# Kernel optimization log

Hardware: AMD Instinct MI355X
Metric: run time of the kernel (lower is better)

## Reference

```python
import jax, jax.numpy as jnp
import numpy as np
from jax import lax

B, T, C_IN, H, K = 8, 4096, 256, 256, 3


def _conv1d_same(x_nct, w_oik, b_o):
    # x: [B, C, T], w: [H, C, K], b: [H] -> [B, H, T], 'same' padding
    y = lax.conv_general_dilated(x_nct, w_oik, window_strides=(1,),
                                 padding='SAME',
                                 dimension_numbers=('NCH', 'OIH', 'NCH'))
    return y + b_o[None, :, None]


def setup_inputs() -> dict:
    key = jax.random.key(0)
    ks = jax.random.split(key, 7)
    std = 1.0 / np.sqrt(H)
    u = lambda k, shape: jax.random.uniform(k, shape, jnp.float32, -std, std)
    return {
        'inputs': jax.random.normal(ks[0], (B, T, C_IN), jnp.float32),
        'init_f': jax.random.normal(ks[1], (B, H), jnp.float32),
        'init_z': jax.random.normal(ks[2], (B, H), jnp.float32),
        'f_w': u(ks[3], (H, C_IN, K)),
        'f_b': u(ks[4], (H,)),
        'z_w': u(ks[5], (H, C_IN, K)),
        'z_b': u(ks[6], (H,)),
    }


def reference(inputs, init_f, init_z, f_w, f_b, z_w, z_b):
    x = jnp.transpose(inputs, (0, 2, 1))                    # [B, C, T]
    raw_f = jnp.transpose(_conv1d_same(x, f_w, f_b), (0, 2, 1))  # [B, T, H]
    raw_z = jnp.transpose(_conv1d_same(x, z_w, z_b), (0, 2, 1))
    # prepend init state along time: init_state[0] -> f, init_state[1] -> z
    raw_f = jnp.concatenate([init_f[:, None, :], raw_f], axis=1)  # [B, T+1, H]
    raw_z = jnp.concatenate([init_z[:, None, :], raw_z], axis=1)
    log_one_minus_f = jax.nn.log_sigmoid(-raw_f)
    log_z = jax.nn.log_sigmoid(raw_z)
    log_f = jax.nn.log_sigmoid(raw_f)
    cs = jnp.cumsum(log_f, axis=1)
    recurrent_gates = log_f - cs + cs[:, -1:, :]
    log_hidden = lax.cumlogsumexp(log_z + log_one_minus_f + recurrent_gates, axis=1)
    return jnp.exp(log_hidden - recurrent_gates)            # [B, T+1, H]
```

## Files before the change

kernel.cpp:

```cpp
#include <hip/hip_runtime.h>
#include <hip/hip_bf16.h>

#define B_ 8
#define T_ 4096
#define C_ 256
#define H_ 256
#define K_ 3
#define NC 128
#define TC 32
#define WFRAG_ELEMS (24 * 32 * 64 * 8)

typedef __attribute__((ext_vector_type(8))) __bf16 bf16x8;
typedef __attribute__((ext_vector_type(4))) float f32x4;

__device__ __forceinline__ float sigm(float x) { return 1.0f / (1.0f + __expf(-x)); }

__device__ __forceinline__ ushort f2bf(float f) {
    union { float f; unsigned u; } v; v.f = f;
    return (ushort)((v.u + 0x7FFFu + ((v.u >> 16) & 1u)) >> 16);
}
__device__ __forceinline__ float bf2f(ushort u) {
    union { unsigned u; float f; } v; v.u = ((unsigned)u) << 16; return v.f;
}
__device__ __forceinline__ unsigned cvt_pk_bf16(float lo, float hi) {
    unsigned r;
    asm("v_cvt_pk_bf16_f32 %0, %1, %2" : "=v"(r) : "v"(lo), "v"(hi));
    return r;
}

__global__ __launch_bounds__(256) void wfrag_kernel(const float* __restrict__ fw,
                                                    const float* __restrict__ zw,
                                                    ushort* __restrict__ wfrag) {
    int idx = blockIdx.x * 256 + threadIdx.x;
    if (idx >= WFRAG_ELEMS) return;
    int j   = idx & 7;
    int l   = (idx >> 3) & 63;
    int ntg = (idx >> 9) & 31;
    int ks  = idx >> 14;
    int n = ntg * 16 + (l & 15);
    int kappa = ks * 32 + (l >> 4) * 8 + j;
    int k = kappa >> 8, c = kappa & 255;
    const float* w = (n < 256) ? fw : zw;
    int h = n & 255;
    wfrag[idx] = f2bf(w[(h * C_ + c) * K_ + k]);
}

__device__ __forceinline__ void bload(const ushort* wb, int ks, const int (&ntg)[4],
                                      bf16x8 (&dst)[4]) {
#pragma unroll
    for (int ni = 0; ni < 4; ++ni)
        dst[ni] = *(const bf16x8*)(wb + (size_t)ks * 16384 + (size_t)ntg[ni] * 512);
}

__device__ __forceinline__ void conv_step(const char* smem, int ks, int lr, int lg,
                                          const bf16x8 (&bfr)[4], f32x4 (&acc)[4][4]) {
    const int k = ks >> 3;
    const int cb = ((ks & 7) * 32 + lg * 8) * 2;
    bf16x8 afr[4];
#pragma unroll
    for (int mi = 0; mi < 4; ++mi) {
        int row = mi * 16 + lr + k;
        afr[mi] = *(const bf16x8*)(smem + row * 512 + (cb ^ ((row & 7) << 4)));
    }
    __builtin_amdgcn_s_setprio(1);
#pragma unroll
    for (int ni = 0; ni < 4; ++ni)
#pragma unroll
        for (int mi = 0; mi < 4; ++mi)
            acc[mi][ni] = __builtin_amdgcn_mfma_f32_16x16x32_bf16(afr[mi], bfr[ni], acc[mi][ni], 0, 0, 0);
    __builtin_amdgcn_s_setprio(0);
}

__global__ __launch_bounds__(512, 4) void conv_scan_kernel(const float* __restrict__ x,
                                                           const ushort* __restrict__ wfrag,
                                                           const float* __restrict__ fb,
                                                           const float* __restrict__ zb,
                                                           unsigned* __restrict__ AP,
                                                           float2* __restrict__ ab) {
    __shared__ __align__(16) char smem[65536];
    unsigned* buf = (unsigned*)smem;

    const int b = blockIdx.y;
    const int t0 = blockIdx.x * 64;
    const int tid = threadIdx.x;

    if (blockIdx.x == 0 || blockIdx.x == gridDim.x - 1) {
        for (int idx = tid; idx < 66 * 64; idx += 512) {
            int row = idx >> 6;
            int c4 = (idx & 63) * 4;
            int t = t0 - 1 + row;
            float4 v = make_float4(0.f, 0.f, 0.f, 0.f);
            if (t >= 0 && t < T_) v = *(const float4*)(x + ((size_t)(b * T_ + t)) * C_ + c4);
            uint2 w2 = make_uint2(cvt_pk_bf16(v.x, v.y), cvt_pk_bf16(v.z, v.w));
            *(uint2*)(smem + row * 512 + ((c4 * 2) ^ ((row & 7) << 4))) = w2;
        }
    } else {
        for (int idx = tid; idx < 66 * 64; idx += 512) {
            int row = idx >> 6;
            int c4 = (idx & 63) * 4;
            int t = t0 - 1 + row;
            float4 v = *(const float4*)(x + ((size_t)(b * T_ + t)) * C_ + c4);
            uint2 w2 = make_uint2(cvt_pk_bf16(v.x, v.y), cvt_pk_bf16(v.z, v.w));
            *(uint2*)(smem + row * 512 + ((c4 * 2) ^ ((row & 7) << 4))) = w2;
        }
    }
    __syncthreads();

    const int wv = tid >> 6;
    const int l  = tid & 63;
    const int lr = l & 15;
    const int lg = l >> 4;
    const int h0 = wv * 32;

    f32x4 acc[4][4];
#pragma unroll
    for (int ni = 0; ni < 4; ++ni) {
        float bv = (ni < 2 ? fb : zb)[h0 + (ni & 1) * 16 + lr];
        f32x4 bvv = {bv, bv, bv, bv};
#pragma unroll
        for (int mi = 0; mi < 4; ++mi) acc[mi][ni] = bvv;
    }

    const ushort* wb = wfrag + (size_t)l * 8;
    int ntg_[4];
#pragma unroll
    for (int ni = 0; ni < 4; ++ni)
        ntg_[ni] = (ni < 2) ? (wv * 2 + ni) : (16 + wv * 2 + ni - 2);

    bf16x8 ba[4], bb[4];
    bload(wb, 0, ntg_, ba);
#pragma unroll 1
    for (int ks = 0; ks < 24; ks += 2) {
        bload(wb, ks + 1, ntg_, bb);
        conv_step(smem, ks, lr, lg, ba, acc);
        if (ks + 2 < 24) bload(wb, ks + 2, ntg_, ba);
        conv_step(smem, ks + 1, lr, lg, bb, acc);
    }

    __syncthreads();
#pragma unroll
    for (int mi = 0; mi < 4; ++mi) {
#pragma unroll
        for (int ni = 0; ni < 2; ++ni) {
            const int h = h0 + ni * 16 + lr;
#pragma unroll
            for (int r = 0; r < 4; ++r) {
                float fv = sigm(acc[mi][ni][r]);
                float av = sigm(acc[mi][ni + 2][r]) * (1.0f - fv);
                int tl = (mi & 1) * 16 + lg * 4 + r;
                int trow = (mi >> 1) * 32 + tl;
                buf[trow * 256 + (h ^ ((tl << 2) & 31))] = cvt_pk_bf16(av, fv);
            }
        }
    }
    __syncthreads();

    {
        const int ch = tid >> 8;
        const int h = tid & 255;
        const int chunk = blockIdx.x * 2 + ch;
        const int r0 = chunk * TC;
        const unsigned* bp = buf + ch * 32 * 256;
        unsigned* app = AP + ((size_t)b * T_ + r0) * H_ + h;
        unsigned u = bp[h];
        float A = bf2f((ushort)(u & 0xffff));
        float Pp = 1.0f;
        float f_prev = bf2f((ushort)(u >> 16));
        app[0] = cvt_pk_bf16(A, Pp);
#pragma unroll 8
        for (int j = 1; j < TC; ++j) {
            u = bp[j * 256 + (h ^ ((j << 2) & 31))];
            float a = bf2f((ushort)(u & 0xffff));
            float f = bf2f((ushort)(u >> 16));
            A = fmaf(f_prev, A, a);
            Pp *= f_prev;
            f_prev = f;
            app[(size_t)j * H_] = cvt_pk_bf16(A, Pp);
        }
        ab[((size_t)b * NC + chunk) * H_ + h] = make_float2(f_prev * A, f_prev * Pp);
    }
}

__global__ __launch_bounds__(256) void chainapply_kernel(const unsigned* __restrict__ AP,
                                                         const float2* __restrict__ ab,
                                                         const float* __restrict__ init_f,
                                                         const float* __restrict__ init_z,
                                                         float* __restrict__ out) {
    const int p = blockIdx.x;
    const int tq = p >> 3;
    const int c = 16 * (tq >> 1) + 2 * (p & 7) + (tq & 1);
    const int b = blockIdx.y;
    const int h = threadIdx.x;

    float f0 = sigm(init_f[b * H_ + h]);
    float z0 = sigm(init_z[b * H_ + h]);
    float s0 = z0 * (1.0f - f0);
    if (c == 0) out[(size_t)b * (T_ + 1) * H_ + h] = s0;

    float uv = f0 * s0;
    const float2* abp = ab + (size_t)b * NC * H_ + h;
#pragma unroll 8
    for (int cc = 0; cc < c; ++cc) {
        float2 q = abp[(size_t)cc * H_];
        uv = fmaf(q.y, uv, q.x);
    }

    const unsigned* app = AP + ((size_t)b * T_ + c * TC) * H_ + h;
    float* op = out + ((size_t)b * (T_ + 1) + c * TC + 1) * H_ + h;
#pragma unroll 8
    for (int j = 0; j < TC; ++j) {
        unsigned w = app[(size_t)j * H_];
        op[(size_t)j * H_] = fmaf(bf2f((ushort)(w >> 16)), uv, bf2f((ushort)(w & 0xffff)));
    }
}

extern "C" void kernel_launch(void* const* d_in, const int* in_sizes, int n_in,
                              void* d_out, int out_size, void* d_ws, size_t ws_size,
                              hipStream_t stream) {
    const float* inputs = (const float*)d_in[0];
    const float* init_f = (const float*)d_in[1];
    const float* init_z = (const float*)d_in[2];
    const float* f_w    = (const float*)d_in[3];
    const float* f_b    = (const float*)d_in[4];
    const float* z_w    = (const float*)d_in[5];
    const float* z_b    = (const float*)d_in[6];
    float* out = (float*)d_out;

    ushort* wfrag = (ushort*)d_ws;
    unsigned* AP  = (unsigned*)(wfrag + WFRAG_ELEMS);
    float2* ab    = (float2*)(AP + (size_t)B_ * T_ * H_);

    wfrag_kernel<<<(WFRAG_ELEMS + 255) / 256, 256, 0, stream>>>(f_w, z_w, wfrag);

    dim3 cgrid(T_ / 64, B_, 1);
    conv_scan_kernel<<<cgrid, 512, 0, stream>>>(inputs, wfrag, f_b, z_b, AP, ab);

    dim3 agrid(NC, B_, 1);
    chainapply_kernel<<<agrid, 256, 0, stream>>>(AP, ab, init_f, init_z, out);
}
```

Baseline: 64.79 us.

## Double conv tile to 128 timesteps per block to reuse weight fragments

Each conv block now processes 128 timesteps with two accumulator sets, so every weight fragment loaded from global feeds twice as many MFMAs. The epilogue scans the result in two passes through shared memory, and chainapply's chunk ordering is remapped to match. Dynamic shared memory grows to hold the larger input halo. The cost is more accumulator registers and lower occupancy (launch bound 2), plus a grid of only 256 blocks, which may underfill the GPU.

```diff
diff --git a/kernel.cpp b/kernel.cpp
--- a/kernel.cpp
+++ b/kernel.cpp
@@ -8,7 +8,9 @@
 #define K_ 3
 #define NC 128
 #define TC 32
+#define BM 128
 #define WFRAG_ELEMS (24 * 32 * 64 * 8)
+#define SMEM_BYTES 66560
 
 typedef __attribute__((ext_vector_type(8))) __bf16 bf16x8;
 typedef __attribute__((ext_vector_type(4))) float f32x4;
@@ -52,40 +54,46 @@
         dst[ni] = *(const bf16x8*)(wb + (size_t)ks * 16384 + (size_t)ntg[ni] * 512);
 }
 
-__device__ __forceinline__ void conv_step(const char* smem, int ks, int lr, int lg,
-                                          const bf16x8 (&bfr)[4], f32x4 (&acc)[4][4]) {
+__device__ __forceinline__ void conv_step2(const char* smem, int ks, int lr, int lg,
+                                           const bf16x8 (&bfr)[4], f32x4 (&acc)[2][4][4]) {
     const int k = ks >> 3;
     const int cb = ((ks & 7) * 32 + lg * 8) * 2;
-    bf16x8 afr[4];
-#pragma unroll
-    for (int mi = 0; mi < 4; ++mi) {
-        int row = mi * 16 + lr + k;
-        afr[mi] = *(const bf16x8*)(smem + row * 512 + (cb ^ ((row & 7) << 4)));
-    }
+    bf16x8 afr[2][4];
+#pragma unroll
+    for (int tt = 0; tt < 2; ++tt)
+#pragma unroll
+        for (int mi = 0; mi < 4; ++mi) {
+            int row = tt * 64 + mi * 16 + lr + k;
+            afr[tt][mi] = *(const bf16x8*)(smem + row * 512 + (cb ^ ((row & 7) << 4)));
+        }
     __builtin_amdgcn_s_setprio(1);
 #pragma unroll
     for (int ni = 0; ni < 4; ++ni)
 #pragma unroll
-        for (int mi = 0; mi < 4; ++mi)
-            acc[mi][ni] = __builtin_amdgcn_mfma_f32_16x16x32_bf16(afr[mi], bfr[ni], acc[mi][ni], 0, 0, 0);
+        for (int tt = 0; tt < 2; ++tt)
+#pragma unroll
+            for (int mi = 0; mi < 4; ++mi)
+                acc[tt][mi][ni] = __builtin_amdgcn_mfma_f32_16x16x32_bf16(afr[tt][mi], bfr[ni],
+                                                                          acc[tt][mi][ni], 0, 0, 0);
     __builtin_amdgcn_s_setprio(0);
 }
 
-__global__ __launch_bounds__(512, 4) void conv_scan_kernel(const float* __restrict__ x,
+__global__ __launch_bounds__(512, 2) void conv_scan_kernel(const float* __restrict__ x,
                                                            const ushort* __restrict__ wfrag,
                                                            const float* __restrict__ fb,
                                                            const float* __restrict__ zb,
                                                            unsigned* __restrict__ AP,
                                                            float2* __restrict__ ab) {
-    __shared__ __align__(16) char smem[65536];
+    extern __shared__ __align__(16) char smem[];
     unsigned* buf = (unsigned*)smem;
 
     const int b = blockIdx.y;
-    const int t0 = blockIdx.x * 64;
+    const int bx = blockIdx.x;
+    const int t0 = bx * BM;
     const int tid = threadIdx.x;
 
-    if (blockIdx.x == 0 || blockIdx.x == gridDim.x - 1) {
-        for (int idx = tid; idx < 66 * 64; idx += 512) {
+    if (bx == 0 || bx == gridDim.x - 1) {
+        for (int idx = tid; idx < 130 * 64; idx += 512) {
             int row = idx >> 6;
             int c4 = (idx & 63) * 4;
             int t = t0 - 1 + row;
@@ -95,7 +103,7 @@
             *(uint2*)(smem + row * 512 + ((c4 * 2) ^ ((row & 7) << 4))) = w2;
         }
     } else {
-        for (int idx = tid; idx < 66 * 64; idx += 512) {
+        for (int idx = tid; idx < 130 * 64; idx += 512) {
             int row = idx >> 6;
             int c4 = (idx & 63) * 4;
             int t = t0 - 1 + row;
@@ -112,13 +120,15 @@
     const int lg = l >> 4;
     const int h0 = wv * 32;
 
-    f32x4 acc[4][4];
+    f32x4 acc[2][4][4];
 #pragma unroll
     for (int ni = 0; ni < 4; ++ni) {
         float bv = (ni < 2 ? fb : zb)[h0 + (ni & 1) * 16 + lr];
         f32x4 bvv = {bv, bv, bv, bv};
 #pragma unroll
-        for (int mi = 0; mi < 4; ++mi) acc[mi][ni] = bvv;
+        for (int tt = 0; tt < 2; ++tt)
+#pragma unroll
+            for (int mi = 0; mi < 4; ++mi) acc[tt][mi][ni] = bvv;
     }
 
     const ushort* wb = wfrag + (size_t)l * 8;
@@ -132,33 +142,34 @@
 #pragma unroll 1
     for (int ks = 0; ks < 24; ks += 2) {
         bload(wb, ks + 1, ntg_, bb);
-        conv_step(smem, ks, lr, lg, ba, acc);
+        conv_step2(smem, ks, lr, lg, ba, acc);
         if (ks + 2 < 24) bload(wb, ks + 2, ntg_, ba);
-        conv_step(smem, ks + 1, lr, lg, bb, acc);
-    }
-
-    __syncthreads();
-#pragma unroll
-    for (int mi = 0; mi < 4; ++mi) {
-#pragma unroll
-        for (int ni = 0; ni < 2; ++ni) {
-            const int h = h0 + ni * 16 + lr;
-#pragma unroll
-            for (int r = 0; r < 4; ++r) {
-                float fv = sigm(acc[mi][ni][r]);
-                float av = sigm(acc[mi][ni + 2][r]) * (1.0f - fv);
-                int tl = (mi & 1) * 16 + lg * 4 + r;
-                int trow = (mi >> 1) * 32 + tl;
-                buf[trow * 256 + (h ^ ((tl << 2) & 31))] = cvt_pk_bf16(av, fv);
+        conv_step2(smem, ks + 1, lr, lg, bb, acc);
+    }
+
+#pragma unroll 1
+    for (int p = 0; p < 2; ++p) {
+        __syncthreads();
+#pragma unroll
+        for (int mi = 0; mi < 4; ++mi) {
+#pragma unroll
+            for (int ni = 0; ni < 2; ++ni) {
+                const int h = h0 + ni * 16 + lr;
+#pragma unroll
+                for (int r = 0; r < 4; ++r) {
+                    float fv = sigm(acc[p][mi][ni][r]);
+                    float av = sigm(acc[p][mi][ni + 2][r]) * (1.0f - fv);
+                    int tl = (mi & 1) * 16 + lg * 4 + r;
+                    int trow = (mi >> 1) * 32 + tl;
+                    buf[trow * 256 + (h ^ ((tl << 2) & 31))] = cvt_pk_bf16(av, fv);
+                }
             }
         }
-    }
-    __syncthreads();
-
-    {
+        __syncthreads();
+
         const int ch = tid >> 8;
         const int h = tid & 255;
-        const int chunk = blockIdx.x * 2 + ch;
+        const int chunk = bx * 4 + 2 * p + ch;
         const int r0 = chunk * TC;
         const unsigned* bp = buf + ch * 32 * 256;
         unsigned* app = AP + ((size_t)b * T_ + r0) * H_ + h;
@@ -187,8 +198,8 @@
                                                          const float* __restrict__ init_z,
                                                          float* __restrict__ out) {
     const int p = blockIdx.x;
-    const int tq = p >> 3;
-    const int c = 16 * (tq >> 1) + 2 * (p & 7) + (tq & 1);
+    const int q = p >> 3;
+    const int c = 4 * ((p & 7) + 8 * (q >> 2)) + (q & 3);
     const int b = blockIdx.y;
     const int h = threadIdx.x;
 
@@ -201,8 +212,8 @@
     const float2* abp = ab + (size_t)b * NC * H_ + h;
 #pragma unroll 8
     for (int cc = 0; cc < c; ++cc) {
-        float2 q = abp[(size_t)cc * H_];
-        uv = fmaf(q.y, uv, q.x);
+        float2 qv = abp[(size_t)cc * H_];
+        uv = fmaf(qv.y, uv, qv.x);
     }
 
     const unsigned* app = AP + ((size_t)b * T_ + c * TC) * H_ + h;
@@ -232,8 +243,10 @@
 
     wfrag_kernel<<<(WFRAG_ELEMS + 255) / 256, 256, 0, stream>>>(f_w, z_w, wfrag);
 
-    dim3 cgrid(T_ / 64, B_, 1);
-    conv_scan_kernel<<<cgrid, 512, 0, stream>>>(inputs, wfrag, f_b, z_b, AP, ab);
+    hipFuncSetAttribute((const void*)conv_scan_kernel,
+                        hipFuncAttributeMaxDynamicSharedMemorySize, SMEM_BYTES);
+    dim3 cgrid(T_ / BM, B_, 1);
+    conv_scan_kernel<<<cgrid, 512, SMEM_BYTES, stream>>>(inputs, wfrag, f_b, z_b, AP, ab);
 
     dim3 agrid(NC, B_, 1);
     chainapply_kernel<<<agrid, 256, 0, stream>>>(AP, ab, init_f, init_z, out);
```

New measurement: 85.02 us. 1.31x slower.

## Split conv-scan blocks across hidden halves and software-pipeline LDS A loads

Applied to the files above, without the earlier changes.

The conv+scan kernel now runs with 256 threads per block and a third grid dimension that splits the hidden units into two halves. This doubles the block count and shrinks shared memory to the 66-row input tile, allowing more resident blocks. The A-fragment LDS loads are double-buffered alongside the B loads so they overlap the MFMAs. The epilogue and per-chunk scan run in two phases that reuse the smaller buffer. Each time tile of input is now loaded and converted twice (once per half), and only 128 of 256 threads take part in the scan.

```diff
diff --git a/kernel.cpp b/kernel.cpp
--- a/kernel.cpp
+++ b/kernel.cpp
@@ -52,16 +52,19 @@
         dst[ni] = *(const bf16x8*)(wb + (size_t)ks * 16384 + (size_t)ntg[ni] * 512);
 }
 
-__device__ __forceinline__ void conv_step(const char* smem, int ks, int lr, int lg,
-                                          const bf16x8 (&bfr)[4], f32x4 (&acc)[4][4]) {
+__device__ __forceinline__ void aload(const char* smem, int ks, int lr, int lg,
+                                      bf16x8 (&afr)[4]) {
     const int k = ks >> 3;
     const int cb = ((ks & 7) * 32 + lg * 8) * 2;
-    bf16x8 afr[4];
 #pragma unroll
     for (int mi = 0; mi < 4; ++mi) {
         int row = mi * 16 + lr + k;
         afr[mi] = *(const bf16x8*)(smem + row * 512 + (cb ^ ((row & 7) << 4)));
     }
+}
+
+__device__ __forceinline__ void mfma_step(const bf16x8 (&afr)[4], const bf16x8 (&bfr)[4],
+                                          f32x4 (&acc)[4][4]) {
     __builtin_amdgcn_s_setprio(1);
 #pragma unroll
     for (int ni = 0; ni < 4; ++ni)
@@ -71,21 +74,70 @@
     __builtin_amdgcn_s_setprio(0);
 }
 
-__global__ __launch_bounds__(512, 4) void conv_scan_kernel(const float* __restrict__ x,
+template <int P>
+__device__ __forceinline__ void epi_write(f32x4 (&acc)[4][4], unsigned* buf,
+                                          int lr, int lg, int h0l) {
+#pragma unroll
+    for (int m2 = 0; m2 < 2; ++m2) {
+        const int mi = 2 * P + m2;
+#pragma unroll
+        for (int ni = 0; ni < 2; ++ni) {
+            const int hl = h0l + ni * 16 + lr;
+#pragma unroll
+            for (int r = 0; r < 4; ++r) {
+                float fv = sigm(acc[mi][ni][r]);
+                float av = sigm(acc[mi][ni + 2][r]) * (1.0f - fv);
+                int tl = m2 * 16 + lg * 4 + r;
+                buf[tl * 128 + (hl ^ ((tl << 2) & 31))] = cvt_pk_bf16(av, fv);
+            }
+        }
+    }
+}
+
+template <int P>
+__device__ __forceinline__ void chunk_scan(const unsigned* buf, int b, int bx, int hh,
+                                           int tid, unsigned* AP, float2* ab) {
+    if (tid < 128) {
+        const int hl = tid;
+        const int hg = hh * 128 + hl;
+        const int chunk = bx * 2 + P;
+        unsigned* app = AP + ((size_t)b * T_ + chunk * TC) * H_ + hg;
+        unsigned u = buf[hl];
+        float A = bf2f((ushort)(u & 0xffff));
+        float Pp = 1.0f;
+        float f_prev = bf2f((ushort)(u >> 16));
+        app[0] = cvt_pk_bf16(A, Pp);
+#pragma unroll 8
+        for (int j = 1; j < TC; ++j) {
+            u = buf[j * 128 + (hl ^ ((j << 2) & 31))];
+            float a = bf2f((ushort)(u & 0xffff));
+            float f = bf2f((ushort)(u >> 16));
+            A = fmaf(f_prev, A, a);
+            Pp *= f_prev;
+            f_prev = f;
+            app[(size_t)j * H_] = cvt_pk_bf16(A, Pp);
+        }
+        ab[((size_t)b * NC + chunk) * H_ + hg] = make_float2(f_prev * A, f_prev * Pp);
+    }
+}
+
+__global__ __launch_bounds__(256, 3) void conv_scan_kernel(const float* __restrict__ x,
                                                            const ushort* __restrict__ wfrag,
                                                            const float* __restrict__ fb,
                                                            const float* __restrict__ zb,
                                                            unsigned* __restrict__ AP,
                                                            float2* __restrict__ ab) {
-    __shared__ __align__(16) char smem[65536];
+    __shared__ __align__(16) char smem[66 * 512];
     unsigned* buf = (unsigned*)smem;
 
     const int b = blockIdx.y;
-    const int t0 = blockIdx.x * 64;
+    const int bx = blockIdx.x;
+    const int hh = blockIdx.z;
+    const int t0 = bx * 64;
     const int tid = threadIdx.x;
 
-    if (blockIdx.x == 0 || blockIdx.x == gridDim.x - 1) {
-        for (int idx = tid; idx < 66 * 64; idx += 512) {
+    if (bx == 0 || bx == gridDim.x - 1) {
+        for (int idx = tid; idx < 66 * 64; idx += 256) {
             int row = idx >> 6;
             int c4 = (idx & 63) * 4;
             int t = t0 - 1 + row;
@@ -95,7 +147,7 @@
             *(uint2*)(smem + row * 512 + ((c4 * 2) ^ ((row & 7) << 4))) = w2;
         }
     } else {
-        for (int idx = tid; idx < 66 * 64; idx += 512) {
+        for (int idx = tid; idx < 66 * 64; idx += 256) {
             int row = idx >> 6;
             int c4 = (idx & 63) * 4;
             int t = t0 - 1 + row;
@@ -110,12 +162,13 @@
     const int l  = tid & 63;
     const int lr = l & 15;
     const int lg = l >> 4;
-    const int h0 = wv * 32;
+    const int h0l = wv * 32;
+    const int h0g = hh * 128 + h0l;
 
     f32x4 acc[4][4];
 #pragma unroll
     for (int ni = 0; ni < 4; ++ni) {
-        float bv = (ni < 2 ? fb : zb)[h0 + (ni & 1) * 16 + lr];
+        float bv = (ni < 2 ? fb : zb)[h0g + (ni & 1) * 16 + lr];
         f32x4 bvv = {bv, bv, bv, bv};
 #pragma unroll
         for (int mi = 0; mi < 4; ++mi) acc[mi][ni] = bvv;
@@ -125,60 +178,32 @@
     int ntg_[4];
 #pragma unroll
     for (int ni = 0; ni < 4; ++ni)
-        ntg_[ni] = (ni < 2) ? (wv * 2 + ni) : (16 + wv * 2 + ni - 2);
-
-    bf16x8 ba[4], bb[4];
+        ntg_[ni] = (ni < 2) ? (hh * 8 + wv * 2 + ni) : (16 + hh * 8 + wv * 2 + ni - 2);
+
+    bf16x8 aA[4], aB[4], ba[4], bb[4];
     bload(wb, 0, ntg_, ba);
+    aload(smem, 0, lr, lg, aA);
 #pragma unroll 1
     for (int ks = 0; ks < 24; ks += 2) {
         bload(wb, ks + 1, ntg_, bb);
-        conv_step(smem, ks, lr, lg, ba, acc);
-        if (ks + 2 < 24) bload(wb, ks + 2, ntg_, ba);
-        conv_step(smem, ks + 1, lr, lg, bb, acc);
-    }
-
-    __syncthreads();
-#pragma unroll
-    for (int mi = 0; mi < 4; ++mi) {
-#pragma unroll
-        for (int ni = 0; ni < 2; ++ni) {
-            const int h = h0 + ni * 16 + lr;
-#pragma unroll
-            for (int r = 0; r < 4; ++r) {
-                float fv = sigm(acc[mi][ni][r]);
-                float av = sigm(acc[mi][ni + 2][r]) * (1.0f - fv);
-                int tl = (mi & 1) * 16 + lg * 4 + r;
-                int trow = (mi >> 1) * 32 + tl;
-                buf[trow * 256 + (h ^ ((tl << 2) & 31))] = cvt_pk_bf16(av, fv);
-            }
-        }
-    }
-    __syncthreads();
-
-    {
-        const int ch = tid >> 8;
-        const int h = tid & 255;
-        const int chunk = blockIdx.x * 2 + ch;
-        const int r0 = chunk * TC;
-        const unsigned* bp = buf + ch * 32 * 256;
-        unsigned* app = AP + ((size_t)b * T_ + r0) * H_ + h;
-        unsigned u = bp[h];
-        float A = bf2f((ushort)(u & 0xffff));
-        float Pp = 1.0f;
-        float f_prev = bf2f((ushort)(u >> 16));
-        app[0] = cvt_pk_bf16(A, Pp);
-#pragma unroll 8
-        for (int j = 1; j < TC; ++j) {
-            u = bp[j * 256 + (h ^ ((j << 2) & 31))];
-            float a = bf2f((ushort)(u & 0xffff));
-            float f = bf2f((ushort)(u >> 16));
-            A = fmaf(f_prev, A, a);
-            Pp *= f_prev;
-            f_prev = f;
-            app[(size_t)j * H_] = cvt_pk_bf16(A, Pp);
-        }
-        ab[((size_t)b * NC + chunk) * H_ + h] = make_float2(f_prev * A, f_prev * Pp);
-    }
+        aload(smem, ks + 1, lr, lg, aB);
+        mfma_step(aA, ba, acc);
+        if (ks + 2 < 24) {
+            bload(wb, ks + 2, ntg_, ba);
+            aload(smem, ks + 2, lr, lg, aA);
+        }
+        mfma_step(aB, bb, acc);
+    }
+
+    __syncthreads();
+    epi_write<0>(acc, buf, lr, lg, h0l);
+    __syncthreads();
+    chunk_scan<0>(buf, b, bx, hh, tid, AP, ab);
+
+    __syncthreads();
+    epi_write<1>(acc, buf, lr, lg, h0l);
+    __syncthreads();
+    chunk_scan<1>(buf, b, bx, hh, tid, AP, ab);
 }
 
 __global__ __launch_bounds__(256) void chainapply_kernel(const unsigned* __restrict__ AP,
@@ -201,8 +226,8 @@
     const float2* abp = ab + (size_t)b * NC * H_ + h;
 #pragma unroll 8
     for (int cc = 0; cc < c; ++cc) {
-        float2 q = abp[(size_t)cc * H_];
-        uv = fmaf(q.y, uv, q.x);
+        float2 qv = abp[(size_t)cc * H_];
+        uv = fmaf(qv.y, uv, qv.x);
     }
 
     const unsigned* app = AP + ((size_t)b * T_ + c * TC) * H_ + h;
@@ -232,8 +257,8 @@
 
     wfrag_kernel<<<(WFRAG_ELEMS + 255) / 256, 256, 0, stream>>>(f_w, z_w, wfrag);
 
-    dim3 cgrid(T_ / 64, B_, 1);
-    conv_scan_kernel<<<cgrid, 512, 0, stream>>>(inputs, wfrag, f_b, z_b, AP, ab);
+    dim3 cgrid(T_ / 64, B_, 2);
+    conv_scan_kernel<<<cgrid, 256, 0, stream>>>(inputs, wfrag, f_b, z_b, AP, ab);
 
     dim3 agrid(NC, B_, 1);
     chainapply_kernel<<<agrid, 256, 0, stream>>>(AP, ab, init_f, init_z, out);
```

Measured after the change: 70.67 us. +9.1%, slower.
